# Performance work log

Measured on AMD Instinct MI355X. Metric: run time of the kernel, lower is better.

Reference implementation:

```python
import jax, jax.numpy as jnp
import numpy as np


def _mlp(x, W1, b1, W2, b2):
    # x: (B, M, T); torch MLPLayer: transpose(1,2) -> Linear -> Linear -> LeakyReLU -> transpose back
    h = jnp.einsum('bmt,hm->bht', x, W1) + b1[None, :, None]   # (B, H, T)
    y = jnp.einsum('bht,oh->bot', h, W2) + b2[None, :, None]   # (B, M, T)
    return jax.nn.leaky_relu(y, negative_slope=0.01)


def _calc_attn(q, k, v):
    # q: (B, M, Tq), k: (B, M, Tk), v: (B, M, Tk)
    Tq = q.shape[-1]
    qk = jnp.einsum('bmq,bmk->bqk', q, k)                       # (B, Tq, Tk)
    eye = jnp.eye(Tq, dtype=qk.dtype)                           # broadcasts: (Tq,Tq) or (1,1)
    logits = jnp.exp(qk - qk * eye / jnp.sqrt(jnp.asarray(Tq, qk.dtype)))
    scores = jax.nn.softmax(logits, axis=-1)
    return jnp.einsum('bqk,bmk->bmq', scores, v)                # (B, M, Tq)


def setup_inputs() -> dict:
    key = jax.random.key(0)
    B, M, T, H = 16, 128, 2048, 512
    ks = jax.random.split(key, 14)
    s = 0.02
    inp = {
        'pattern': jax.random.normal(ks[0], (B, M, T), jnp.float32),
        'value': jax.random.normal(ks[1], (B, M, T), jnp.float32),
        'kernel_size': 33,
    }
    names = ['q', 'k', 'o']
    for i, n in enumerate(names):
        inp['W%s1' % n] = jax.random.normal(ks[2 + 4 * i], (H, M), jnp.float32) * s
        inp['b%s1' % n] = jax.random.normal(ks[3 + 4 * i], (H,), jnp.float32) * s
        inp['W%s2' % n] = jax.random.normal(ks[4 + 4 * i], (M, H), jnp.float32) * s
        inp['b%s2' % n] = jax.random.normal(ks[5 + 4 * i], (M,), jnp.float32) * s
    return inp


def reference(pattern, value, kernel_size, Wq1, bq1, Wq2, bq2, Wk1, bk1, Wk2, bk2, Wo1, bo1, Wo2, bo2):
    query = _mlp(pattern, Wq1, bq1, Wq2, bq2)
    key = _mlp(pattern, Wk1, bk1, Wk2, bk2)
    # full (internal) attention
    attn_in = _calc_attn(query, key, value)                     # (B, M, T)
    rep_in = _mlp(attn_in, Wo1, bo1, Wo2, bo2)
    # windowed (external) attention
    T = query.shape[-1]
    cu = (kernel_size - 1) // 2
    q_w = query[..., T - 1 - cu : T - cu]                       # (B, M, 1)
    k_w = key[..., kernel_size - cu - 1 : T - cu - 2]           # (B, M, T-k-1)
    v_w = value[..., kernel_size : T - 1]                       # (B, M, T-k-1)
    attn_ex = _calc_attn(q_w, k_w, v_w)                         # (B, M, 1)
    rep_ex = _mlp(attn_ex, Wo1, bo1, Wo2, bo2)
    return jnp.concatenate([rep_in, rep_ex], axis=-1)           # (B, M, T+1)
```

## Files before the change

### kernel.cpp

```cpp
#include <hip/hip_runtime.h>
#include <hip/hip_bf16.h>
#include <math.h>

#define B_    16
#define M_    128
#define T_    2048
#define H_    512
#define TOUT_ 2049

typedef unsigned short u16;
typedef unsigned int   u32;
typedef __bf16 bf16x8 __attribute__((ext_vector_type(8)));
typedef float  f32x16 __attribute__((ext_vector_type(16)));
typedef float  f32x4  __attribute__((ext_vector_type(4)));
typedef u32    u32x4  __attribute__((ext_vector_type(4)));
typedef u32    u32x2  __attribute__((ext_vector_type(2)));

#define A_OFF     0
#define C_OFF     16384
#define MEAN_OFF  16896
#define AQKBF_OFF 19200
#define AOBF_OFF  35584
#define QT_OFF    43776
#define KT_OFF    (43776 + 2097152)
#define VB_OFF    (43776 + 2 * 2097152)

static __device__ __forceinline__ u16 f2bf(float f) {
  u32 u = __float_as_uint(f);
  u = (u + 0x7FFFu + ((u >> 16) & 1u)) >> 16;
  return (u16)u;
}
static __device__ __forceinline__ u32 pk2(float lo, float hi) {
  __hip_bfloat162 h = __float22bfloat162_rn(float2{lo, hi});
  u32 r;
  __builtin_memcpy(&r, &h, 4);
  return r;
}
static __device__ __forceinline__ bf16x8 ldfrag(const u16* p) {
  return __builtin_bit_cast(bf16x8, *(const u32x4*)p);
}
static __device__ __forceinline__ float ex2(float x) {
#if __has_builtin(__builtin_amdgcn_exp2f)
  return __builtin_amdgcn_exp2f(x);
#else
  return exp2f(x);
#endif
}

__global__ __launch_bounds__(128) void fuse_weights_all(
    const float* __restrict__ W1q, const float* __restrict__ b1q,
    const float* __restrict__ W2q, const float* __restrict__ b2q,
    const float* __restrict__ W1k, const float* __restrict__ b1k,
    const float* __restrict__ W2k, const float* __restrict__ b2k,
    const float* __restrict__ W1o, const float* __restrict__ b1o,
    const float* __restrict__ W2o, const float* __restrict__ b2o,
    float* __restrict__ A, float* __restrict__ c,
    u16* __restrict__ Aqk_bf, u16* __restrict__ Ao_bf) {
  __shared__ float w2row[H_];
  int which = blockIdx.x >> 7;
  int o = blockIdx.x & 127;
  const float* W1 = which == 0 ? W1q : which == 1 ? W1k : W1o;
  const float* b1 = which == 0 ? b1q : which == 1 ? b1k : b1o;
  const float* W2 = which == 0 ? W2q : which == 1 ? W2k : W2o;
  const float* b2 = which == 0 ? b2q : which == 1 ? b2k : b2o;
  int m = threadIdx.x;
  for (int h = m; h < H_; h += 128) w2row[h] = W2[o * H_ + h];
  __syncthreads();
  float acc = 0.f;
#pragma unroll 8
  for (int h = 0; h < H_; ++h) acc = fmaf(w2row[h], W1[h * M_ + m], acc);
  u16 ab = f2bf(acc);
  if (which == 0)      Aqk_bf[o * 128 + m] = ab;
  else if (which == 1) Aqk_bf[(128 + o) * 128 + m] = ab;
  else               { Ao_bf[o * 128 + m] = ab; A[o * M_ + m] = acc; }
  if (m < 64) {
    float cc = 0.f;
    for (int h = m; h < H_; h += 64) cc = fmaf(w2row[h], b1[h], cc);
#pragma unroll
    for (int off = 32; off > 0; off >>= 1) cc += __shfl_down(cc, off, 64);
    if (m == 0) c[which * 128 + o] = cc + b2[o];
  }
}

#define XS 68

__global__ __launch_bounds__(256) void prep_kernel(
    const float* __restrict__ pattern, const u16* __restrict__ Aqk_bf,
    const float* __restrict__ cqk, u16* __restrict__ qT, u16* __restrict__ kT,
    const float* __restrict__ value, u16* __restrict__ vb,
    float* __restrict__ meanv) {
  __shared__ alignas(16) float xsf[128 * XS];
  int bx = blockIdx.x;
  int tid = threadIdx.x;

  if (bx >= 512) {
    int bm = bx - 512;
    float* red = xsf;
    const float* row = value + (size_t)bm * T_;
    int i0 = tid * 8;
    float4 a = *(const float4*)(row + i0);
    float4 bq = *(const float4*)(row + i0 + 4);
    u32x4 o = {pk2(a.x, a.y), pk2(a.z, a.w), pk2(bq.x, bq.y), pk2(bq.z, bq.w)};
    *(u32x4*)&vb[(size_t)bm * T_ + i0] = o;
    float vals[8] = {a.x, a.y, a.z, a.w, bq.x, bq.y, bq.z, bq.w};
    float s = 0.f;
#pragma unroll
    for (int j = 0; j < 8; ++j) {
      int idx = i0 + j;
      if (idx >= 33 && idx < T_ - 1) s += vals[j];
    }
    red[tid] = s;
    __syncthreads();
    for (int st = 128; st > 0; st >>= 1) {
      if (tid < st) red[tid] += red[tid + st];
      __syncthreads();
    }
    if (tid == 0) meanv[bm] = red[0] * (1.f / 2014.f);
    return;
  }

  int b = bx >> 5;
  int t0 = (bx & 31) * 64;
  int lane = tid & 63;
  int wv = tid >> 6;
  int l31 = lane & 31;
  int lh8 = (lane >> 5) * 8;

  bf16x8 afr[2][8];
#pragma unroll
  for (int i = 0; i < 2; ++i) {
    const u16* ap = Aqk_bf + ((2 * wv + i) * 32 + l31) * 128 + lh8;
#pragma unroll
    for (int s = 0; s < 8; ++s) afr[i][s] = ldfrag(ap + 16 * s);
  }

#pragma unroll
  for (int rep = 0; rep < 8; ++rep) {
    int m = rep * 16 + (tid >> 4);
    int tc = (tid & 15) * 4;
    float4 v = *(const float4*)&pattern[(size_t)(b * M_ + m) * T_ + t0 + tc];
    *(float4*)&xsf[m * XS + tc] = v;
  }
  __syncthreads();

  bf16x8 bfr[2][8];
#pragma unroll
  for (int tt = 0; tt < 2; ++tt) {
#pragma unroll
    for (int s = 0; s < 8; ++s) {
      float v0 = xsf[(s * 16 + lh8 + 0) * XS + tt * 32 + l31];
      float v1 = xsf[(s * 16 + lh8 + 1) * XS + tt * 32 + l31];
      float v2 = xsf[(s * 16 + lh8 + 2) * XS + tt * 32 + l31];
      float v3 = xsf[(s * 16 + lh8 + 3) * XS + tt * 32 + l31];
      float v4 = xsf[(s * 16 + lh8 + 4) * XS + tt * 32 + l31];
      float v5 = xsf[(s * 16 + lh8 + 5) * XS + tt * 32 + l31];
      float v6 = xsf[(s * 16 + lh8 + 6) * XS + tt * 32 + l31];
      float v7 = xsf[(s * 16 + lh8 + 7) * XS + tt * 32 + l31];
      u32x4 p = {pk2(v0, v1), pk2(v2, v3), pk2(v4, v5), pk2(v6, v7)};
      bfr[tt][s] = __builtin_bit_cast(bf16x8, p);
    }
  }
  __syncthreads();

  u16* obuf = (u16*)xsf;
#pragma unroll
  for (int tt = 0; tt < 2; ++tt) {
#pragma unroll
    for (int i = 0; i < 2; ++i) {
      f32x16 acc;
#pragma unroll
      for (int r = 0; r < 16; ++r) acc[r] = 0.f;
#pragma unroll
      for (int s = 0; s < 8; ++s)
        acc = __builtin_amdgcn_mfma_f32_32x32x16_bf16(afr[i][s], bfr[tt][s], acc, 0, 0, 0);
      int ot = 2 * wv + i;
      int t = tt * 32 + l31;
      float sc = (ot < 4) ? 1.44269504f : 1.0f;
#pragma unroll
      for (int r = 0; r < 16; ++r) {
        int orow = (r & 3) + 8 * (r >> 2) + 4 * (lane >> 5);
        float v = acc[r] + cqk[ot * 32 + orow];
        v = v > 0.f ? v : 0.01f * v;
        obuf[t * 258 + ot * 32 + orow] = f2bf(v * sc);
      }
    }
  }
  __syncthreads();

  const u32* ob32 = (const u32*)obuf;
#pragma unroll
  for (int g = 0; g < 8; ++g) {
    int G = wv * 8 + g;
    int mat = G >> 4;
    int t = (G & 15) * 4 + (lane >> 4);
    int og2 = lane & 15;
    int wbase = t * 129 + mat * 64 + og2 * 4;
    u32x4 vv = {ob32[wbase], ob32[wbase + 1], ob32[wbase + 2], ob32[wbase + 3]};
    u32* dst = (u32*)((mat ? kT : qT) + ((size_t)(b * T_ + t0 + t)) * 128) + og2 * 4;
    *(u32x4*)dst = vv;
  }
}

#define QSTR 136
#define VSTR 72
#define NKT  (T_ / 64)
#define CINIT 0.52876637f

__global__ __launch_bounds__(256, 2) void attn_mfma_kernel(
    const u16* __restrict__ qT, const u16* __restrict__ kT,
    const u16* __restrict__ vB, const u16* __restrict__ Ao_bf,
    const float* __restrict__ co, const float* __restrict__ Aofp,
    const float* __restrict__ meanv, float* __restrict__ out) {
  extern __shared__ u16 smem[];
  u16* ks0 = smem;
  u16* ks1 = ks0 + 64 * QSTR;
  u16* vs0 = ks1 + 64 * QSTR;
  u16* vs1 = vs0 + 128 * VSTR;
  float* dls  = (float*)(vs1 + 128 * VSTR);
  float* pbuf = (float*)ks0;
  u16*   ptbuf = vs0;

  int b = blockIdx.y;
  int q0 = blockIdx.x * 64;
  int tid = threadIdx.x;
  int lane = tid & 63;
  int wv = tid >> 6;
  int l31 = lane & 31;
  int h = lane >> 5;
  int lh8 = h * 8;
  int qt = wv & 1;
  int kh = wv >> 1;

  const u16* gkb = kT + (size_t)b * T_ * 128;
  const u16* gvb = vB + (size_t)b * M_ * T_;
  int kr = tid >> 4, kc = (tid & 15) * 8;
  int vr = tid >> 3, vc = (tid & 7) * 8;

  u32x4 kreg[4], vreg[4];
#pragma unroll
  for (int it = 0; it < 4; ++it) {
    kreg[it] = *(const u32x4*)&gkb[(size_t)(it * 16 + kr) * 128 + kc];
    vreg[it] = *(const u32x4*)&gvb[(size_t)(it * 32 + vr) * T_ + vc];
  }

  bf16x8 qfrag[8];
  {
    const u16* qrow = qT + (size_t)(b * T_ + q0 + qt * 32 + l31) * 128 + lh8;
#pragma unroll
    for (int s = 0; s < 8; ++s) qfrag[s] = ldfrag(qrow + s * 16);
  }

#pragma unroll
  for (int it = 0; it < 4; ++it) {
    *(u32x4*)&ks0[(it * 16 + kr) * QSTR + kc] = kreg[it];
    *(u32x4*)&vs0[(it * 32 + vr) * VSTR + vc] = vreg[it];
  }
#pragma unroll
  for (int it = 0; it < 4; ++it) {
    kreg[it] = *(const u32x4*)&gkb[(size_t)(64 + it * 16 + kr) * 128 + kc];
    vreg[it] = *(const u32x4*)&gvb[(size_t)(it * 32 + vr) * T_ + 64 + vc];
  }

  f32x16 pacc[4];
  float den = 0.f;
#pragma unroll
  for (int i = 0; i < 16; ++i) {
    pacc[0][i] = 0.f; pacc[1][i] = 0.f; pacc[2][i] = 0.f; pacc[3][i] = 0.f;
  }

  for (int kt = 0; kt < NKT; ++kt) {
    int k0 = kt * 64;
    u16* kcur = (kt & 1) ? ks1 : ks0;
    u16* knxt = (kt & 1) ? ks0 : ks1;
    u16* vcur = (kt & 1) ? vs1 : vs0;
    u16* vnxt = (kt & 1) ? vs0 : vs1;
    __syncthreads();

    f32x16 sacc;
#pragma unroll
    for (int i = 0; i < 16; ++i) sacc[i] = CINIT;
    {
      const u16* krow = &kcur[(kh * 32 + l31) * QSTR + lh8];
      __builtin_amdgcn_s_setprio(1);
#pragma unroll
      for (int s = 0; s < 8; ++s) {
        bf16x8 kf = ldfrag(krow + s * 16);
        sacc = __builtin_amdgcn_mfma_f32_32x32x16_bf16(kf, qfrag[s], sacc, 0, 0, 0);
      }
      __builtin_amdgcn_s_setprio(0);
    }

    if (kt < NKT - 1) {
#pragma unroll
      for (int it = 0; it < 4; ++it) {
        *(u32x4*)&knxt[(it * 16 + kr) * QSTR + kc] = kreg[it];
        *(u32x4*)&vnxt[(it * 32 + vr) * VSTR + vc] = vreg[it];
      }
      int kn = (kt + 2 < NKT) ? (kt + 2) * 64 : (NKT - 1) * 64;
#pragma unroll
      for (int it = 0; it < 4; ++it) {
        kreg[it] = *(const u32x4*)&gkb[(size_t)(kn + it * 16 + kr) * 128 + kc];
        vreg[it] = *(const u32x4*)&gvb[(size_t)(it * 32 + vr) * T_ + kn + vc];
      }
    }

    if (k0 + kh * 32 == q0 + qt * 32) {
#pragma unroll
      for (int r = 0; r < 16; ++r) {
        int row = (r & 3) + 8 * (r >> 2) + 4 * h;
        if (row == l31) sacc[r] = fmaf(sacc[r], 0.97790291f, 0.01168420f);
      }
    }

    float w[16];
#pragma unroll
    for (int r = 0; r < 16; ++r) w[r] = ex2(ex2(sacc[r]));
    {
      float d0 = (w[0] + w[1]) + (w[2] + w[3]);
      float d1 = (w[4] + w[5]) + (w[6] + w[7]);
      float d2 = (w[8] + w[9]) + (w[10] + w[11]);
      float d3 = (w[12] + w[13]) + (w[14] + w[15]);
      den += (d0 + d1) + (d2 + d3);
    }
    u32 p00 = pk2(w[0], w[1]),  p01 = pk2(w[2], w[3]);
    u32 p10 = pk2(w[4], w[5]),  p11 = pk2(w[6], w[7]);
    u32 p20 = pk2(w[8], w[9]),  p21 = pk2(w[10], w[11]);
    u32 p30 = pk2(w[12], w[13]), p31 = pk2(w[14], w[15]);
    u32 e0 = __shfl_xor(h ? p00 : p10, 32, 64);
    u32 e1 = __shfl_xor(h ? p01 : p11, 32, 64);
    u32 e2 = __shfl_xor(h ? p20 : p30, 32, 64);
    u32 e3 = __shfl_xor(h ? p21 : p31, 32, 64);
    u32x4 f0 = h ? u32x4{e0, e1, p10, p11} : u32x4{p00, p01, e0, e1};
    u32x4 f1 = h ? u32x4{e2, e3, p30, p31} : u32x4{p20, p21, e2, e3};
    bf16x8 bw0 = __builtin_bit_cast(bf16x8, f0);
    bf16x8 bw1 = __builtin_bit_cast(bf16x8, f1);

    __builtin_amdgcn_s_setprio(1);
#pragma unroll
    for (int mt = 0; mt < 4; ++mt) {
      const u16* vrow = &vcur[(mt * 32 + l31) * VSTR + kh * 32 + lh8];
      bf16x8 vf0 = ldfrag(vrow);
      bf16x8 vf1 = ldfrag(vrow + 16);
      pacc[mt] = __builtin_amdgcn_mfma_f32_32x32x16_bf16(vf0, bw0, pacc[mt], 0, 0, 0);
      pacc[mt] = __builtin_amdgcn_mfma_f32_32x32x16_bf16(vf1, bw1, pacc[mt], 0, 0, 0);
    }
    __builtin_amdgcn_s_setprio(0);
  }

  float dq = den + __shfl_xor(den, 32, 64);

  __syncthreads();

  if (kh == 1) {
#pragma unroll
    for (int mt = 0; mt < 4; ++mt) {
      float* pb = &pbuf[((size_t)(qt * 4 + mt) * 64 + lane) * 16];
#pragma unroll
      for (int g = 0; g < 4; ++g) {
        f32x4 v = {pacc[mt][4 * g], pacc[mt][4 * g + 1],
                   pacc[mt][4 * g + 2], pacc[mt][4 * g + 3]};
        *(f32x4*)(pb + 4 * g) = v;
      }
    }
    if (lane < 32) dls[qt * 32 + lane] = dq;
  }
  __syncthreads();

  if (kh == 0) {
    float rden = 1.f / (dq + dls[qt * 32 + l31]);
#pragma unroll
    for (int mt = 0; mt < 4; ++mt) {
      const float* pb = &pbuf[((size_t)(qt * 4 + mt) * 64 + lane) * 16];
#pragma unroll
      for (int g = 0; g < 4; ++g) {
        f32x4 t = *(const f32x4*)(pb + 4 * g);
        float v0 = (pacc[mt][4 * g + 0] + t[0]) * rden;
        float v1 = (pacc[mt][4 * g + 1] + t[1]) * rden;
        float v2 = (pacc[mt][4 * g + 2] + t[2]) * rden;
        float v3 = (pacc[mt][4 * g + 3] + t[3]) * rden;
        int m0 = mt * 32 + 8 * g + 4 * h;
        u32x2 wp = {pk2(v0, v1), pk2(v2, v3)};
        *(u32x2*)&ptbuf[(qt * 32 + l31) * QSTR + m0] = wp;
      }
    }
  }
  __syncthreads();

  bf16x8 aofr[8];
  {
    const u16* ap = Ao_bf + (wv * 32 + l31) * 128 + lh8;
#pragma unroll
    for (int s = 0; s < 8; ++s) aofr[s] = ldfrag(ap + 16 * s);
  }
#pragma unroll
  for (int j = 0; j < 2; ++j) {
    bf16x8 pfr[8];
    const u16* pp = &ptbuf[(j * 32 + l31) * QSTR + lh8];
#pragma unroll
    for (int s = 0; s < 8; ++s) pfr[s] = ldfrag(pp + 16 * s);
    f32x16 oacc;
#pragma unroll
    for (int r = 0; r < 16; ++r) oacc[r] = 0.f;
#pragma unroll
    for (int s = 0; s < 8; ++s)
      oacc = __builtin_amdgcn_mfma_f32_32x32x16_bf16(aofr[s], pfr[s], oacc, 0, 0, 0);
#pragma unroll
    for (int r = 0; r < 16; ++r) {
      int orow = wv * 32 + (r & 3) + 8 * (r >> 2) + 4 * h;
      float v = oacc[r] + co[orow];
      v = v > 0.f ? v : 0.01f * v;
      out[((size_t)(b * M_ + orow)) * TOUT_ + q0 + j * 32 + l31] = v;
    }
  }

  if (blockIdx.x == 0 && tid < 128) {
    float acc = co[tid];
    const float* mv = meanv + b * 128;
    for (int m = 0; m < 128; ++m) acc = fmaf(Aofp[tid * 128 + m], mv[m], acc);
    acc = acc > 0.f ? acc : 0.01f * acc;
    out[((size_t)(b * M_ + tid)) * TOUT_ + 2048] = acc;
  }
}

extern "C" void kernel_launch(void* const* d_in, const int* in_sizes, int n_in,
                              void* d_out, int out_size, void* d_ws, size_t ws_size,
                              hipStream_t stream) {
  (void)in_sizes; (void)n_in; (void)out_size; (void)ws_size;
  const float* pattern = (const float*)d_in[0];
  const float* value   = (const float*)d_in[1];
  const float* Wq1 = (const float*)d_in[3];
  const float* bq1 = (const float*)d_in[4];
  const float* Wq2 = (const float*)d_in[5];
  const float* bq2 = (const float*)d_in[6];
  const float* Wk1 = (const float*)d_in[7];
  const float* bk1 = (const float*)d_in[8];
  const float* Wk2 = (const float*)d_in[9];
  const float* bk2 = (const float*)d_in[10];
  const float* Wo1 = (const float*)d_in[11];
  const float* bo1 = (const float*)d_in[12];
  const float* Wo2 = (const float*)d_in[13];
  const float* bo2 = (const float*)d_in[14];

  float* ws     = (float*)d_ws;
  float* A      = ws + A_OFF;
  float* c      = ws + C_OFF;
  float* meanv  = ws + MEAN_OFF;
  u16*   Aqk_bf = (u16*)(ws + AQKBF_OFF);
  u16*   Ao_bf  = (u16*)(ws + AOBF_OFF);
  u16*   qT     = (u16*)(ws + QT_OFF);
  u16*   kT     = (u16*)(ws + KT_OFF);
  u16*   vB     = (u16*)(ws + VB_OFF);
  float* out    = (float*)d_out;

  fuse_weights_all<<<384, 128, 0, stream>>>(
      Wq1, bq1, Wq2, bq2, Wk1, bk1, Wk2, bk2, Wo1, bo1, Wo2, bo2,
      A, c, Aqk_bf, Ao_bf);

  prep_kernel<<<512 + B_ * M_, 256, 0, stream>>>(
      pattern, Aqk_bf, c, qT, kT, value, vB, meanv);

  size_t lds_bytes = (size_t)(2 * 64 * QSTR + 2 * 128 * VSTR) * 2 + 64 * 4;
  attn_mfma_kernel<<<dim3(T_ / 64, B_), 256, lds_bytes, stream>>>(
      qT, kT, vB, Ao_bf, c + 256, A, meanv, out);
}
```

Baseline: 196.9 us.

## Double attention query/key tile to 128 with 512-thread blocks

The attention kernel now processes 128 queries per block with 8 waves, and each loop iteration covers 128 keys. Each wave computes two 32x32 score tiles per step. This halves how often K/V tiles are streamed per query and gives more independent MFMA work in each iteration. In exchange, LDS use roughly doubles, so only one block fits per CU. The grid shrinks to 256 blocks, and register pressure under launch_bounds(512,2) may force spills.

Measured after the change: 190.1 us. -3.4%, faster.

```diff
diff --git a/kernel.cpp b/kernel.cpp
--- a/kernel.cpp
+++ b/kernel.cpp
@@ -202,46 +202,39 @@
 }
 
 #define QSTR 136
-#define VSTR 72
-#define NKT  (T_ / 64)
+#define VSTR 136
+#define KTILE 128
+#define NKT  (T_ / KTILE)
 #define CINIT 0.52876637f
 
-__global__ __launch_bounds__(256, 2) void attn_mfma_kernel(
+__global__ __launch_bounds__(512, 2) void attn_mfma_kernel(
     const u16* __restrict__ qT, const u16* __restrict__ kT,
     const u16* __restrict__ vB, const u16* __restrict__ Ao_bf,
     const float* __restrict__ co, const float* __restrict__ Aofp,
     const float* __restrict__ meanv, float* __restrict__ out) {
   extern __shared__ u16 smem[];
   u16* ks0 = smem;
-  u16* ks1 = ks0 + 64 * QSTR;
-  u16* vs0 = ks1 + 64 * QSTR;
+  u16* ks1 = ks0 + 128 * QSTR;
+  u16* vs0 = ks1 + 128 * QSTR;
   u16* vs1 = vs0 + 128 * VSTR;
   float* dls  = (float*)(vs1 + 128 * VSTR);
   float* pbuf = (float*)ks0;
   u16*   ptbuf = vs0;
 
   int b = blockIdx.y;
-  int q0 = blockIdx.x * 64;
+  int q0 = blockIdx.x * 128;
   int tid = threadIdx.x;
   int lane = tid & 63;
   int wv = tid >> 6;
   int l31 = lane & 31;
   int h = lane >> 5;
   int lh8 = h * 8;
-  int qt = wv & 1;
-  int kh = wv >> 1;
+  int qt = wv & 3;
+  int kh = wv >> 2;
 
   const u16* gkb = kT + (size_t)b * T_ * 128;
   const u16* gvb = vB + (size_t)b * M_ * T_;
   int kr = tid >> 4, kc = (tid & 15) * 8;
-  int vr = tid >> 3, vc = (tid & 7) * 8;
-
-  u32x4 kreg[4], vreg[4];
-#pragma unroll
-  for (int it = 0; it < 4; ++it) {
-    kreg[it] = *(const u32x4*)&gkb[(size_t)(it * 16 + kr) * 128 + kc];
-    vreg[it] = *(const u32x4*)&gvb[(size_t)(it * 32 + vr) * T_ + vc];
-  }
 
   bf16x8 qfrag[8];
   {
@@ -250,15 +243,21 @@
     for (int s = 0; s < 8; ++s) qfrag[s] = ldfrag(qrow + s * 16);
   }
 
+  u32x4 kreg[4], vreg[4];
 #pragma unroll
   for (int it = 0; it < 4; ++it) {
-    *(u32x4*)&ks0[(it * 16 + kr) * QSTR + kc] = kreg[it];
-    *(u32x4*)&vs0[(it * 32 + vr) * VSTR + vc] = vreg[it];
+    kreg[it] = *(const u32x4*)&gkb[(size_t)(it * 32 + kr) * 128 + kc];
+    vreg[it] = *(const u32x4*)&gvb[(size_t)(it * 32 + kr) * T_ + kc];
   }
 #pragma unroll
   for (int it = 0; it < 4; ++it) {
-    kreg[it] = *(const u32x4*)&gkb[(size_t)(64 + it * 16 + kr) * 128 + kc];
-    vreg[it] = *(const u32x4*)&gvb[(size_t)(it * 32 + vr) * T_ + 64 + vc];
+    *(u32x4*)&ks0[(it * 32 + kr) * QSTR + kc] = kreg[it];
+    *(u32x4*)&vs0[(it * 32 + kr) * VSTR + kc] = vreg[it];
+  }
+#pragma unroll
+  for (int it = 0; it < 4; ++it) {
+    kreg[it] = *(const u32x4*)&gkb[(size_t)(KTILE + it * 32 + kr) * 128 + kc];
+    vreg[it] = *(const u32x4*)&gvb[(size_t)(it * 32 + kr) * T_ + KTILE + kc];
   }
 
   f32x16 pacc[4];
@@ -269,23 +268,29 @@
   }
 
   for (int kt = 0; kt < NKT; ++kt) {
-    int k0 = kt * 64;
+    int k0 = kt * KTILE;
     u16* kcur = (kt & 1) ? ks1 : ks0;
     u16* knxt = (kt & 1) ? ks0 : ks1;
     u16* vcur = (kt & 1) ? vs1 : vs0;
     u16* vnxt = (kt & 1) ? vs0 : vs1;
     __syncthreads();
 
-    f32x16 sacc;
-#pragma unroll
-    for (int i = 0; i < 16; ++i) sacc[i] = CINIT;
+    f32x16 sacc_a, sacc_b;
+#pragma unroll
+    for (int i = 0; i < 16; ++i) { sacc_a[i] = CINIT; sacc_b[i] = CINIT; }
     {
-      const u16* krow = &kcur[(kh * 32 + l31) * QSTR + lh8];
+      const u16* krowa = &kcur[(kh * 64 + l31) * QSTR + lh8];
+      const u16* krowb = krowa + 32 * QSTR;
       __builtin_amdgcn_s_setprio(1);
 #pragma unroll
       for (int s = 0; s < 8; ++s) {
-        bf16x8 kf = ldfrag(krow + s * 16);
-        sacc = __builtin_amdgcn_mfma_f32_32x32x16_bf16(kf, qfrag[s], sacc, 0, 0, 0);
+        bf16x8 kfa = ldfrag(krowa + s * 16);
+        sacc_a = __builtin_amdgcn_mfma_f32_32x32x16_bf16(kfa, qfrag[s], sacc_a, 0, 0, 0);
+      }
+#pragma unroll
+      for (int s = 0; s < 8; ++s) {
+        bf16x8 kfb = ldfrag(krowb + s * 16);
+        sacc_b = __builtin_amdgcn_mfma_f32_32x32x16_bf16(kfb, qfrag[s], sacc_b, 0, 0, 0);
       }
       __builtin_amdgcn_s_setprio(0);
     }
@@ -293,58 +298,95 @@
     if (kt < NKT - 1) {
 #pragma unroll
       for (int it = 0; it < 4; ++it) {
-        *(u32x4*)&knxt[(it * 16 + kr) * QSTR + kc] = kreg[it];
-        *(u32x4*)&vnxt[(it * 32 + vr) * VSTR + vc] = vreg[it];
-      }
-      int kn = (kt + 2 < NKT) ? (kt + 2) * 64 : (NKT - 1) * 64;
+        *(u32x4*)&knxt[(it * 32 + kr) * QSTR + kc] = kreg[it];
+        *(u32x4*)&vnxt[(it * 32 + kr) * VSTR + kc] = vreg[it];
+      }
+      int kn = (kt + 2 < NKT) ? (kt + 2) * KTILE : (NKT - 1) * KTILE;
 #pragma unroll
       for (int it = 0; it < 4; ++it) {
-        kreg[it] = *(const u32x4*)&gkb[(size_t)(kn + it * 16 + kr) * 128 + kc];
-        vreg[it] = *(const u32x4*)&gvb[(size_t)(it * 32 + vr) * T_ + kn + vc];
-      }
-    }
-
-    if (k0 + kh * 32 == q0 + qt * 32) {
+        kreg[it] = *(const u32x4*)&gkb[(size_t)(kn + it * 32 + kr) * 128 + kc];
+        vreg[it] = *(const u32x4*)&gvb[(size_t)(it * 32 + kr) * T_ + kn + kc];
+      }
+    }
+
+    if (k0 + kh * 64 == q0 + qt * 32) {
 #pragma unroll
       for (int r = 0; r < 16; ++r) {
         int row = (r & 3) + 8 * (r >> 2) + 4 * h;
-        if (row == l31) sacc[r] = fmaf(sacc[r], 0.97790291f, 0.01168420f);
-      }
-    }
-
-    float w[16];
-#pragma unroll
-    for (int r = 0; r < 16; ++r) w[r] = ex2(ex2(sacc[r]));
+        if (row == l31) sacc_a[r] = fmaf(sacc_a[r], 0.97790291f, 0.01168420f);
+      }
+    } else if (k0 + kh * 64 + 32 == q0 + qt * 32) {
+#pragma unroll
+      for (int r = 0; r < 16; ++r) {
+        int row = (r & 3) + 8 * (r >> 2) + 4 * h;
+        if (row == l31) sacc_b[r] = fmaf(sacc_b[r], 0.97790291f, 0.01168420f);
+      }
+    }
+
     {
+      float w[16];
+#pragma unroll
+      for (int r = 0; r < 16; ++r) w[r] = ex2(ex2(sacc_a[r]));
       float d0 = (w[0] + w[1]) + (w[2] + w[3]);
       float d1 = (w[4] + w[5]) + (w[6] + w[7]);
       float d2 = (w[8] + w[9]) + (w[10] + w[11]);
       float d3 = (w[12] + w[13]) + (w[14] + w[15]);
       den += (d0 + d1) + (d2 + d3);
-    }
-    u32 p00 = pk2(w[0], w[1]),  p01 = pk2(w[2], w[3]);
-    u32 p10 = pk2(w[4], w[5]),  p11 = pk2(w[6], w[7]);
-    u32 p20 = pk2(w[8], w[9]),  p21 = pk2(w[10], w[11]);
-    u32 p30 = pk2(w[12], w[13]), p31 = pk2(w[14], w[15]);
-    u32 e0 = __shfl_xor(h ? p00 : p10, 32, 64);
-    u32 e1 = __shfl_xor(h ? p01 : p11, 32, 64);
-    u32 e2 = __shfl_xor(h ? p20 : p30, 32, 64);
-    u32 e3 = __shfl_xor(h ? p21 : p31, 32, 64);
-    u32x4 f0 = h ? u32x4{e0, e1, p10, p11} : u32x4{p00, p01, e0, e1};
-    u32x4 f1 = h ? u32x4{e2, e3, p30, p31} : u32x4{p20, p21, e2, e3};
-    bf16x8 bw0 = __builtin_bit_cast(bf16x8, f0);
-    bf16x8 bw1 = __builtin_bit_cast(bf16x8, f1);
-
-    __builtin_amdgcn_s_setprio(1);
-#pragma unroll
-    for (int mt = 0; mt < 4; ++mt) {
-      const u16* vrow = &vcur[(mt * 32 + l31) * VSTR + kh * 32 + lh8];
-      bf16x8 vf0 = ldfrag(vrow);
-      bf16x8 vf1 = ldfrag(vrow + 16);
-      pacc[mt] = __builtin_amdgcn_mfma_f32_32x32x16_bf16(vf0, bw0, pacc[mt], 0, 0, 0);
-      pacc[mt] = __builtin_amdgcn_mfma_f32_32x32x16_bf16(vf1, bw1, pacc[mt], 0, 0, 0);
-    }
-    __builtin_amdgcn_s_setprio(0);
+      u32 p00 = pk2(w[0], w[1]),  p01 = pk2(w[2], w[3]);
+      u32 p10 = pk2(w[4], w[5]),  p11 = pk2(w[6], w[7]);
+      u32 p20 = pk2(w[8], w[9]),  p21 = pk2(w[10], w[11]);
+      u32 p30 = pk2(w[12], w[13]), p31 = pk2(w[14], w[15]);
+      u32 e0 = __shfl_xor(h ? p00 : p10, 32, 64);
+      u32 e1 = __shfl_xor(h ? p01 : p11, 32, 64);
+      u32 e2 = __shfl_xor(h ? p20 : p30, 32, 64);
+      u32 e3 = __shfl_xor(h ? p21 : p31, 32, 64);
+      u32x4 f0 = h ? u32x4{e0, e1, p10, p11} : u32x4{p00, p01, e0, e1};
+      u32x4 f1 = h ? u32x4{e2, e3, p30, p31} : u32x4{p20, p21, e2, e3};
+      bf16x8 bw0 = __builtin_bit_cast(bf16x8, f0);
+      bf16x8 bw1 = __builtin_bit_cast(bf16x8, f1);
+      __builtin_amdgcn_s_setprio(1);
+#pragma unroll
+      for (int mt = 0; mt < 4; ++mt) {
+        const u16* vrow = &vcur[(mt * 32 + l31) * VSTR + kh * 64 + lh8];
+        bf16x8 vf0 = ldfrag(vrow);
+        bf16x8 vf1 = ldfrag(vrow + 16);
+        pacc[mt] = __builtin_amdgcn_mfma_f32_32x32x16_bf16(vf0, bw0, pacc[mt], 0, 0, 0);
+        pacc[mt] = __builtin_amdgcn_mfma_f32_32x32x16_bf16(vf1, bw1, pacc[mt], 0, 0, 0);
+      }
+      __builtin_amdgcn_s_setprio(0);
+    }
+    {
+      float w[16];
+#pragma unroll
+      for (int r = 0; r < 16; ++r) w[r] = ex2(ex2(sacc_b[r]));
+      float d0 = (w[0] + w[1]) + (w[2] + w[3]);
+      float d1 = (w[4] + w[5]) + (w[6] + w[7]);
+      float d2 = (w[8] + w[9]) + (w[10] + w[11]);
+      float d3 = (w[12] + w[13]) + (w[14] + w[15]);
+      den += (d0 + d1) + (d2 + d3);
+      u32 p00 = pk2(w[0], w[1]),  p01 = pk2(w[2], w[3]);
+      u32 p10 = pk2(w[4], w[5]),  p11 = pk2(w[6], w[7]);
+      u32 p20 = pk2(w[8], w[9]),  p21 = pk2(w[10], w[11]);
+      u32 p30 = pk2(w[12], w[13]), p31 = pk2(w[14], w[15]);
+      u32 e0 = __shfl_xor(h ? p00 : p10, 32, 64);
+      u32 e1 = __shfl_xor(h ? p01 : p11, 32, 64);
+      u32 e2 = __shfl_xor(h ? p20 : p30, 32, 64);
+      u32 e3 = __shfl_xor(h ? p21 : p31, 32, 64);
+      u32x4 f0 = h ? u32x4{e0, e1, p10, p11} : u32x4{p00, p01, e0, e1};
+      u32x4 f1 = h ? u32x4{e2, e3, p30, p31} : u32x4{p20, p21, e2, e3};
+      bf16x8 bw2 = __builtin_bit_cast(bf16x8, f0);
+      bf16x8 bw3 = __builtin_bit_cast(bf16x8, f1);
+      __builtin_amdgcn_s_setprio(1);
+#pragma unroll
+      for (int mt = 0; mt < 4; ++mt) {
+        const u16* vrow = &vcur[(mt * 32 + l31) * VSTR + kh * 64 + 32 + lh8];
+        bf16x8 vf2 = ldfrag(vrow);
+        bf16x8 vf3 = ldfrag(vrow + 16);
+        pacc[mt] = __builtin_amdgcn_mfma_f32_32x32x16_bf16(vf2, bw2, pacc[mt], 0, 0, 0);
+        pacc[mt] = __builtin_amdgcn_mfma_f32_32x32x16_bf16(vf3, bw3, pacc[mt], 0, 0, 0);
+      }
+      __builtin_amdgcn_s_setprio(0);
+    }
   }
 
   float dq = den + __shfl_xor(den, 32, 64);
@@ -388,14 +430,15 @@
 
   bf16x8 aofr[8];
   {
-    const u16* ap = Ao_bf + (wv * 32 + l31) * 128 + lh8;
+    const u16* ap = Ao_bf + ((wv & 3) * 32 + l31) * 128 + lh8;
 #pragma unroll
     for (int s = 0; s < 8; ++s) aofr[s] = ldfrag(ap + 16 * s);
   }
 #pragma unroll
   for (int j = 0; j < 2; ++j) {
+    int qt2 = kh * 2 + j;
     bf16x8 pfr[8];
-    const u16* pp = &ptbuf[(j * 32 + l31) * QSTR + lh8];
+    const u16* pp = &ptbuf[(qt2 * 32 + l31) * QSTR + lh8];
 #pragma unroll
     for (int s = 0; s < 8; ++s) pfr[s] = ldfrag(pp + 16 * s);
     f32x16 oacc;
@@ -406,10 +449,10 @@
       oacc = __builtin_amdgcn_mfma_f32_32x32x16_bf16(aofr[s], pfr[s], oacc, 0, 0, 0);
 #pragma unroll
     for (int r = 0; r < 16; ++r) {
-      int orow = wv * 32 + (r & 3) + 8 * (r >> 2) + 4 * h;
+      int orow = (wv & 3) * 32 + (r & 3) + 8 * (r >> 2) + 4 * h;
       float v = oacc[r] + co[orow];
       v = v > 0.f ? v : 0.01f * v;
-      out[((size_t)(b * M_ + orow)) * TOUT_ + q0 + j * 32 + l31] = v;
+      out[((size_t)(b * M_ + orow)) * TOUT_ + q0 + qt2 * 32 + l31] = v;
     }
   }
 
@@ -459,7 +502,7 @@
   prep_kernel<<<512 + B_ * M_, 256, 0, stream>>>(
       pattern, Aqk_bf, c, qT, kT, value, vB, meanv);
 
-  size_t lds_bytes = (size_t)(2 * 64 * QSTR + 2 * 128 * VSTR) * 2 + 64 * 4;
-  attn_mfma_kernel<<<dim3(T_ / 64, B_), 256, lds_bytes, stream>>>(
+  size_t lds_bytes = (size_t)(2 * 128 * QSTR + 2 * 128 * VSTR) * 2 + 128 * 4;
+  attn_mfma_kernel<<<dim3(T_ / 128, B_), 512, lds_bytes, stream>>>(
       qT, kT, vB, Ao_bf, c + 256, A, meanv, out);
 }
```

## Enlarge attention blocks to 128 queries with 16 waves sharing K/V tiles

Applied to the files above, without the earlier changes.

Each attention block now has 1024 threads and covers 128 queries instead of 64. Each K/V tile staged in LDS is therefore reused by four query tiles, halving global K/V traffic per query. The PV accumulation is split across two M-halves, so each score tile's QK^T MFMAs and exponentials are computed twice, by both M-half waves. The s_setprio hints are removed. The grid shrinks to 256 blocks using about 99KB of LDS each, which lowers occupancy, and launch_bounds(1024,4) may pressure registers.

Result: slower. 210.2 us (+6.8%).

```diff
diff --git a/kernel.cpp b/kernel.cpp
--- a/kernel.cpp
+++ b/kernel.cpp
@@ -203,46 +203,41 @@
 
 #define QSTR 136
 #define VSTR 72
-#define NKT  (T_ / 64)
+#define KTILE 64
+#define NKT  (T_ / KTILE)
 #define CINIT 0.52876637f
 
-__global__ __launch_bounds__(256, 2) void attn_mfma_kernel(
+__global__ __launch_bounds__(1024, 4) void attn_mfma_kernel(
     const u16* __restrict__ qT, const u16* __restrict__ kT,
     const u16* __restrict__ vB, const u16* __restrict__ Ao_bf,
     const float* __restrict__ co, const float* __restrict__ Aofp,
     const float* __restrict__ meanv, float* __restrict__ out) {
   extern __shared__ u16 smem[];
   u16* ks0 = smem;
-  u16* ks1 = ks0 + 64 * QSTR;
-  u16* vs0 = ks1 + 64 * QSTR;
-  u16* vs1 = vs0 + 128 * VSTR;
-  float* dls  = (float*)(vs1 + 128 * VSTR);
-  float* pbuf = (float*)ks0;
-  u16*   ptbuf = vs0;
+  u16* ks1 = smem + 8704;
+  u16* vs0 = smem + 17408;
+  u16* vs1 = smem + 26624;
+  float* pbuf  = (float*)smem;
+  u16*   ptbuf = smem + 33024;
+  float* dls   = (float*)(smem + 50432);
 
   int b = blockIdx.y;
-  int q0 = blockIdx.x * 64;
+  int q0 = blockIdx.x * 128;
   int tid = threadIdx.x;
   int lane = tid & 63;
   int wv = tid >> 6;
   int l31 = lane & 31;
   int h = lane >> 5;
   int lh8 = h * 8;
-  int qt = wv & 1;
-  int kh = wv >> 1;
+  int qt = wv & 3;
+  int kh = (wv >> 2) & 1;
+  int mh = wv >> 3;
 
   const u16* gkb = kT + (size_t)b * T_ * 128;
   const u16* gvb = vB + (size_t)b * M_ * T_;
   int kr = tid >> 4, kc = (tid & 15) * 8;
   int vr = tid >> 3, vc = (tid & 7) * 8;
 
-  u32x4 kreg[4], vreg[4];
-#pragma unroll
-  for (int it = 0; it < 4; ++it) {
-    kreg[it] = *(const u32x4*)&gkb[(size_t)(it * 16 + kr) * 128 + kc];
-    vreg[it] = *(const u32x4*)&gvb[(size_t)(it * 32 + vr) * T_ + vc];
-  }
-
   bf16x8 qfrag[8];
   {
     const u16* qrow = qT + (size_t)(b * T_ + q0 + qt * 32 + l31) * 128 + lh8;
@@ -250,61 +245,47 @@
     for (int s = 0; s < 8; ++s) qfrag[s] = ldfrag(qrow + s * 16);
   }
 
-#pragma unroll
-  for (int it = 0; it < 4; ++it) {
-    *(u32x4*)&ks0[(it * 16 + kr) * QSTR + kc] = kreg[it];
-    *(u32x4*)&vs0[(it * 32 + vr) * VSTR + vc] = vreg[it];
-  }
-#pragma unroll
-  for (int it = 0; it < 4; ++it) {
-    kreg[it] = *(const u32x4*)&gkb[(size_t)(64 + it * 16 + kr) * 128 + kc];
-    vreg[it] = *(const u32x4*)&gvb[(size_t)(it * 32 + vr) * T_ + 64 + vc];
-  }
-
-  f32x16 pacc[4];
+  u32x4 kreg, vreg;
+  kreg = *(const u32x4*)&gkb[(size_t)kr * 128 + kc];
+  vreg = *(const u32x4*)&gvb[(size_t)vr * T_ + vc];
+  *(u32x4*)&ks0[kr * QSTR + kc] = kreg;
+  *(u32x4*)&vs0[vr * VSTR + vc] = vreg;
+  kreg = *(const u32x4*)&gkb[(size_t)(KTILE + kr) * 128 + kc];
+  vreg = *(const u32x4*)&gvb[(size_t)vr * T_ + KTILE + vc];
+
+  f32x16 pacc[2];
   float den = 0.f;
 #pragma unroll
-  for (int i = 0; i < 16; ++i) {
-    pacc[0][i] = 0.f; pacc[1][i] = 0.f; pacc[2][i] = 0.f; pacc[3][i] = 0.f;
-  }
+  for (int i = 0; i < 16; ++i) { pacc[0][i] = 0.f; pacc[1][i] = 0.f; }
 
   for (int kt = 0; kt < NKT; ++kt) {
-    int k0 = kt * 64;
     u16* kcur = (kt & 1) ? ks1 : ks0;
     u16* knxt = (kt & 1) ? ks0 : ks1;
     u16* vcur = (kt & 1) ? vs1 : vs0;
     u16* vnxt = (kt & 1) ? vs0 : vs1;
     __syncthreads();
 
+    if (kt < NKT - 1) {
+      *(u32x4*)&knxt[kr * QSTR + kc] = kreg;
+      *(u32x4*)&vnxt[vr * VSTR + vc] = vreg;
+      int kn = (kt + 2 < NKT) ? (kt + 2) * KTILE : (NKT - 1) * KTILE;
+      kreg = *(const u32x4*)&gkb[(size_t)(kn + kr) * 128 + kc];
+      vreg = *(const u32x4*)&gvb[(size_t)vr * T_ + kn + vc];
+    }
+
     f32x16 sacc;
 #pragma unroll
     for (int i = 0; i < 16; ++i) sacc[i] = CINIT;
     {
       const u16* krow = &kcur[(kh * 32 + l31) * QSTR + lh8];
-      __builtin_amdgcn_s_setprio(1);
 #pragma unroll
       for (int s = 0; s < 8; ++s) {
         bf16x8 kf = ldfrag(krow + s * 16);
         sacc = __builtin_amdgcn_mfma_f32_32x32x16_bf16(kf, qfrag[s], sacc, 0, 0, 0);
       }
-      __builtin_amdgcn_s_setprio(0);
-    }
-
-    if (kt < NKT - 1) {
-#pragma unroll
-      for (int it = 0; it < 4; ++it) {
-        *(u32x4*)&knxt[(it * 16 + kr) * QSTR + kc] = kreg[it];
-        *(u32x4*)&vnxt[(it * 32 + vr) * VSTR + vc] = vreg[it];
-      }
-      int kn = (kt + 2 < NKT) ? (kt + 2) * 64 : (NKT - 1) * 64;
-#pragma unroll
-      for (int it = 0; it < 4; ++it) {
-        kreg[it] = *(const u32x4*)&gkb[(size_t)(kn + it * 16 + kr) * 128 + kc];
-        vreg[it] = *(const u32x4*)&gvb[(size_t)(it * 32 + vr) * T_ + kn + vc];
-      }
-    }
-
-    if (k0 + kh * 32 == q0 + qt * 32) {
+    }
+
+    if (kt * KTILE + kh * 32 == q0 + qt * 32) {
 #pragma unroll
       for (int r = 0; r < 16; ++r) {
         int row = (r & 3) + 8 * (r >> 2) + 4 * h;
@@ -335,16 +316,15 @@
     bf16x8 bw0 = __builtin_bit_cast(bf16x8, f0);
     bf16x8 bw1 = __builtin_bit_cast(bf16x8, f1);
 
-    __builtin_amdgcn_s_setprio(1);
-#pragma unroll
-    for (int mt = 0; mt < 4; ++mt) {
-      const u16* vrow = &vcur[(mt * 32 + l31) * VSTR + kh * 32 + lh8];
+#pragma unroll
+    for (int i = 0; i < 2; ++i) {
+      int mtg = mh * 2 + i;
+      const u16* vrow = &vcur[(mtg * 32 + l31) * VSTR + kh * 32 + lh8];
       bf16x8 vf0 = ldfrag(vrow);
       bf16x8 vf1 = ldfrag(vrow + 16);
-      pacc[mt] = __builtin_amdgcn_mfma_f32_32x32x16_bf16(vf0, bw0, pacc[mt], 0, 0, 0);
-      pacc[mt] = __builtin_amdgcn_mfma_f32_32x32x16_bf16(vf1, bw1, pacc[mt], 0, 0, 0);
-    }
-    __builtin_amdgcn_s_setprio(0);
+      pacc[i] = __builtin_amdgcn_mfma_f32_32x32x16_bf16(vf0, bw0, pacc[i], 0, 0, 0);
+      pacc[i] = __builtin_amdgcn_mfma_f32_32x32x16_bf16(vf1, bw1, pacc[i], 0, 0, 0);
+    }
   }
 
   float dq = den + __shfl_xor(den, 32, 64);
@@ -353,32 +333,32 @@
 
   if (kh == 1) {
 #pragma unroll
-    for (int mt = 0; mt < 4; ++mt) {
-      float* pb = &pbuf[((size_t)(qt * 4 + mt) * 64 + lane) * 16];
+    for (int i = 0; i < 2; ++i) {
+      float* pb = &pbuf[(((qt * 2 + mh) * 2 + i) * 64 + lane) * 16];
 #pragma unroll
       for (int g = 0; g < 4; ++g) {
-        f32x4 v = {pacc[mt][4 * g], pacc[mt][4 * g + 1],
-                   pacc[mt][4 * g + 2], pacc[mt][4 * g + 3]};
+        f32x4 v = {pacc[i][4 * g], pacc[i][4 * g + 1],
+                   pacc[i][4 * g + 2], pacc[i][4 * g + 3]};
         *(f32x4*)(pb + 4 * g) = v;
       }
     }
-    if (lane < 32) dls[qt * 32 + lane] = dq;
+    if (mh == 0 && lane < 32) dls[qt * 32 + lane] = dq;
   }
   __syncthreads();
 
   if (kh == 0) {
     float rden = 1.f / (dq + dls[qt * 32 + l31]);
 #pragma unroll
-    for (int mt = 0; mt < 4; ++mt) {
-      const float* pb = &pbuf[((size_t)(qt * 4 + mt) * 64 + lane) * 16];
+    for (int i = 0; i < 2; ++i) {
+      const float* pb = &pbuf[(((qt * 2 + mh) * 2 + i) * 64 + lane) * 16];
 #pragma unroll
       for (int g = 0; g < 4; ++g) {
         f32x4 t = *(const f32x4*)(pb + 4 * g);
-        float v0 = (pacc[mt][4 * g + 0] + t[0]) * rden;
-        float v1 = (pacc[mt][4 * g + 1] + t[1]) * rden;
-        float v2 = (pacc[mt][4 * g + 2] + t[2]) * rden;
-        float v3 = (pacc[mt][4 * g + 3] + t[3]) * rden;
-        int m0 = mt * 32 + 8 * g + 4 * h;
+        float v0 = (pacc[i][4 * g + 0] + t[0]) * rden;
+        float v1 = (pacc[i][4 * g + 1] + t[1]) * rden;
+        float v2 = (pacc[i][4 * g + 2] + t[2]) * rden;
+        float v3 = (pacc[i][4 * g + 3] + t[3]) * rden;
+        int m0 = (mh * 2 + i) * 32 + 8 * g + 4 * h;
         u32x2 wp = {pk2(v0, v1), pk2(v2, v3)};
         *(u32x2*)&ptbuf[(qt * 32 + l31) * QSTR + m0] = wp;
       }
@@ -388,14 +368,14 @@
 
   bf16x8 aofr[8];
   {
-    const u16* ap = Ao_bf + (wv * 32 + l31) * 128 + lh8;
+    const u16* ap = Ao_bf + ((wv & 3) * 32 + l31) * 128 + lh8;
 #pragma unroll
     for (int s = 0; s < 8; ++s) aofr[s] = ldfrag(ap + 16 * s);
   }
-#pragma unroll
-  for (int j = 0; j < 2; ++j) {
+  {
+    int qt2 = wv >> 2;
     bf16x8 pfr[8];
-    const u16* pp = &ptbuf[(j * 32 + l31) * QSTR + lh8];
+    const u16* pp = &ptbuf[(qt2 * 32 + l31) * QSTR + lh8];
 #pragma unroll
     for (int s = 0; s < 8; ++s) pfr[s] = ldfrag(pp + 16 * s);
     f32x16 oacc;
@@ -406,10 +386,10 @@
       oacc = __builtin_amdgcn_mfma_f32_32x32x16_bf16(aofr[s], pfr[s], oacc, 0, 0, 0);
 #pragma unroll
     for (int r = 0; r < 16; ++r) {
-      int orow = wv * 32 + (r & 3) + 8 * (r >> 2) + 4 * h;
+      int orow = (wv & 3) * 32 + (r & 3) + 8 * (r >> 2) + 4 * h;
       float v = oacc[r] + co[orow];
       v = v > 0.f ? v : 0.01f * v;
-      out[((size_t)(b * M_ + orow)) * TOUT_ + q0 + j * 32 + l31] = v;
+      out[((size_t)(b * M_ + orow)) * TOUT_ + q0 + qt2 * 32 + l31] = v;
     }
   }
 
@@ -459,7 +439,7 @@
   prep_kernel<<<512 + B_ * M_, 256, 0, stream>>>(
       pattern, Aqk_bf, c, qT, kT, value, vB, meanv);
 
-  size_t lds_bytes = (size_t)(2 * 64 * QSTR + 2 * 128 * VSTR) * 2 + 64 * 4;
-  attn_mfma_kernel<<<dim3(T_ / 64, B_), 256, lds_bytes, stream>>>(
+  size_t lds_bytes = 101376;
+  attn_mfma_kernel<<<dim3(T_ / 128, B_), 1024, lds_bytes, stream>>>(
       qT, kT, vB, Ao_bf, c + 256, A, meanv, out);
 }
```

## Enlarge attention tiles to 128 queries and 128 keys with 1024-thread blocks

Applied to the files above, without the earlier changes.

The attention kernel now handles 128 queries per block with 16 waves (4 query tiles × 4 key splits) and loads 128-key K/V tiles into LDS, halving the grid. This raises reuse of each K/V tile across more queries and cuts global K/V reloads, at the cost of a two-stage cross-wave reduction of partial outputs and denominators through LDS. It also uses much more LDS per block (~138 KB), so only one block fits per CU, and it drops the s_setprio hints. Prefetch stores are moved before the QK MFMAs.

Measured after the change: 252.0 us. +28.0%, slower.

```diff
diff --git a/kernel.cpp b/kernel.cpp
--- a/kernel.cpp
+++ b/kernel.cpp
@@ -202,46 +202,40 @@
 }
 
 #define QSTR 136
-#define VSTR 72
-#define NKT  (T_ / 64)
+#define VSTR 136
+#define KTILE 128
+#define NKT  (T_ / KTILE)
 #define CINIT 0.52876637f
 
-__global__ __launch_bounds__(256, 2) void attn_mfma_kernel(
+__global__ __launch_bounds__(1024) void attn_mfma_kernel(
     const u16* __restrict__ qT, const u16* __restrict__ kT,
     const u16* __restrict__ vB, const u16* __restrict__ Ao_bf,
     const float* __restrict__ co, const float* __restrict__ Aofp,
     const float* __restrict__ meanv, float* __restrict__ out) {
   extern __shared__ u16 smem[];
   u16* ks0 = smem;
-  u16* ks1 = ks0 + 64 * QSTR;
-  u16* vs0 = ks1 + 64 * QSTR;
-  u16* vs1 = vs0 + 128 * VSTR;
-  float* dls  = (float*)(vs1 + 128 * VSTR);
-  float* pbuf = (float*)ks0;
-  u16*   ptbuf = vs0;
+  u16* ks1 = smem + 17408;
+  u16* vs0 = smem + 34816;
+  u16* vs1 = smem + 52224;
+  float* pbuf  = (float*)smem;
+  u16*   ptbuf = smem + 32768;
+  float* dls   = (float*)(smem + 69632);
 
   int b = blockIdx.y;
-  int q0 = blockIdx.x * 64;
+  int q0 = blockIdx.x * 128;
   int tid = threadIdx.x;
   int lane = tid & 63;
   int wv = tid >> 6;
   int l31 = lane & 31;
   int h = lane >> 5;
   int lh8 = h * 8;
-  int qt = wv & 1;
-  int kh = wv >> 1;
+  int qt = wv & 3;
+  int ks = wv >> 2;
 
   const u16* gkb = kT + (size_t)b * T_ * 128;
   const u16* gvb = vB + (size_t)b * M_ * T_;
-  int kr = tid >> 4, kc = (tid & 15) * 8;
-  int vr = tid >> 3, vc = (tid & 7) * 8;
-
-  u32x4 kreg[4], vreg[4];
-#pragma unroll
-  for (int it = 0; it < 4; ++it) {
-    kreg[it] = *(const u32x4*)&gkb[(size_t)(it * 16 + kr) * 128 + kc];
-    vreg[it] = *(const u32x4*)&gvb[(size_t)(it * 32 + vr) * T_ + vc];
-  }
+  int sr = tid >> 3;
+  int sc = (tid & 7) * 16;
 
   bf16x8 qfrag[8];
   {
@@ -250,16 +244,19 @@
     for (int s = 0; s < 8; ++s) qfrag[s] = ldfrag(qrow + s * 16);
   }
 
-#pragma unroll
-  for (int it = 0; it < 4; ++it) {
-    *(u32x4*)&ks0[(it * 16 + kr) * QSTR + kc] = kreg[it];
-    *(u32x4*)&vs0[(it * 32 + vr) * VSTR + vc] = vreg[it];
-  }
-#pragma unroll
-  for (int it = 0; it < 4; ++it) {
-    kreg[it] = *(const u32x4*)&gkb[(size_t)(64 + it * 16 + kr) * 128 + kc];
-    vreg[it] = *(const u32x4*)&gvb[(size_t)(it * 32 + vr) * T_ + 64 + vc];
-  }
+  u32x4 kreg[2], vreg[2];
+  kreg[0] = *(const u32x4*)&gkb[(size_t)sr * 128 + sc];
+  kreg[1] = *(const u32x4*)&gkb[(size_t)sr * 128 + sc + 8];
+  vreg[0] = *(const u32x4*)&gvb[(size_t)sr * T_ + sc];
+  vreg[1] = *(const u32x4*)&gvb[(size_t)sr * T_ + sc + 8];
+  *(u32x4*)&ks0[sr * QSTR + sc] = kreg[0];
+  *(u32x4*)&ks0[sr * QSTR + sc + 8] = kreg[1];
+  *(u32x4*)&vs0[sr * VSTR + sc] = vreg[0];
+  *(u32x4*)&vs0[sr * VSTR + sc + 8] = vreg[1];
+  kreg[0] = *(const u32x4*)&gkb[(size_t)(KTILE + sr) * 128 + sc];
+  kreg[1] = *(const u32x4*)&gkb[(size_t)(KTILE + sr) * 128 + sc + 8];
+  vreg[0] = *(const u32x4*)&gvb[(size_t)sr * T_ + KTILE + sc];
+  vreg[1] = *(const u32x4*)&gvb[(size_t)sr * T_ + KTILE + sc + 8];
 
   f32x16 pacc[4];
   float den = 0.f;
@@ -269,42 +266,37 @@
   }
 
   for (int kt = 0; kt < NKT; ++kt) {
-    int k0 = kt * 64;
     u16* kcur = (kt & 1) ? ks1 : ks0;
     u16* knxt = (kt & 1) ? ks0 : ks1;
     u16* vcur = (kt & 1) ? vs1 : vs0;
     u16* vnxt = (kt & 1) ? vs0 : vs1;
     __syncthreads();
 
+    if (kt < NKT - 1) {
+      *(u32x4*)&knxt[sr * QSTR + sc] = kreg[0];
+      *(u32x4*)&knxt[sr * QSTR + sc + 8] = kreg[1];
+      *(u32x4*)&vnxt[sr * VSTR + sc] = vreg[0];
+      *(u32x4*)&vnxt[sr * VSTR + sc + 8] = vreg[1];
+      int kn = (kt + 2 < NKT) ? (kt + 2) * KTILE : (NKT - 1) * KTILE;
+      kreg[0] = *(const u32x4*)&gkb[(size_t)(kn + sr) * 128 + sc];
+      kreg[1] = *(const u32x4*)&gkb[(size_t)(kn + sr) * 128 + sc + 8];
+      vreg[0] = *(const u32x4*)&gvb[(size_t)sr * T_ + kn + sc];
+      vreg[1] = *(const u32x4*)&gvb[(size_t)sr * T_ + kn + sc + 8];
+    }
+
     f32x16 sacc;
 #pragma unroll
     for (int i = 0; i < 16; ++i) sacc[i] = CINIT;
     {
-      const u16* krow = &kcur[(kh * 32 + l31) * QSTR + lh8];
-      __builtin_amdgcn_s_setprio(1);
+      const u16* krow = &kcur[(ks * 32 + l31) * QSTR + lh8];
 #pragma unroll
       for (int s = 0; s < 8; ++s) {
         bf16x8 kf = ldfrag(krow + s * 16);
         sacc = __builtin_amdgcn_mfma_f32_32x32x16_bf16(kf, qfrag[s], sacc, 0, 0, 0);
       }
-      __builtin_amdgcn_s_setprio(0);
-    }
-
-    if (kt < NKT - 1) {
-#pragma unroll
-      for (int it = 0; it < 4; ++it) {
-        *(u32x4*)&knxt[(it * 16 + kr) * QSTR + kc] = kreg[it];
-        *(u32x4*)&vnxt[(it * 32 + vr) * VSTR + vc] = vreg[it];
-      }
-      int kn = (kt + 2 < NKT) ? (kt + 2) * 64 : (NKT - 1) * 64;
-#pragma unroll
-      for (int it = 0; it < 4; ++it) {
-        kreg[it] = *(const u32x4*)&gkb[(size_t)(kn + it * 16 + kr) * 128 + kc];
-        vreg[it] = *(const u32x4*)&gvb[(size_t)(it * 32 + vr) * T_ + kn + vc];
-      }
-    }
-
-    if (k0 + kh * 32 == q0 + qt * 32) {
+    }
+
+    if (kt * KTILE + ks * 32 == q0 + qt * 32) {
 #pragma unroll
       for (int r = 0; r < 16; ++r) {
         int row = (r & 3) + 8 * (r >> 2) + 4 * h;
@@ -335,45 +327,77 @@
     bf16x8 bw0 = __builtin_bit_cast(bf16x8, f0);
     bf16x8 bw1 = __builtin_bit_cast(bf16x8, f1);
 
-    __builtin_amdgcn_s_setprio(1);
 #pragma unroll
     for (int mt = 0; mt < 4; ++mt) {
-      const u16* vrow = &vcur[(mt * 32 + l31) * VSTR + kh * 32 + lh8];
+      const u16* vrow = &vcur[(mt * 32 + l31) * VSTR + ks * 32 + lh8];
       bf16x8 vf0 = ldfrag(vrow);
       bf16x8 vf1 = ldfrag(vrow + 16);
       pacc[mt] = __builtin_amdgcn_mfma_f32_32x32x16_bf16(vf0, bw0, pacc[mt], 0, 0, 0);
       pacc[mt] = __builtin_amdgcn_mfma_f32_32x32x16_bf16(vf1, bw1, pacc[mt], 0, 0, 0);
     }
-    __builtin_amdgcn_s_setprio(0);
   }
 
   float dq = den + __shfl_xor(den, 32, 64);
 
   __syncthreads();
 
-  if (kh == 1) {
+  if (ks != 0 && lane < 32) dls[ks * 128 + qt * 32 + l31] = dq;
+  if (ks & 1) {
+    int sidx = ks >> 1;
 #pragma unroll
     for (int mt = 0; mt < 4; ++mt) {
-      float* pb = &pbuf[((size_t)(qt * 4 + mt) * 64 + lane) * 16];
+      float* pb = &pbuf[(((sidx * 4 + qt) * 4 + mt) << 10)];
 #pragma unroll
       for (int g = 0; g < 4; ++g) {
         f32x4 v = {pacc[mt][4 * g], pacc[mt][4 * g + 1],
                    pacc[mt][4 * g + 2], pacc[mt][4 * g + 3]};
-        *(f32x4*)(pb + 4 * g) = v;
-      }
-    }
-    if (lane < 32) dls[qt * 32 + lane] = dq;
-  }
-  __syncthreads();
-
-  if (kh == 0) {
-    float rden = 1.f / (dq + dls[qt * 32 + l31]);
+        *(f32x4*)(pb + (g << 8) + lane * 4) = v;
+      }
+    }
+  }
+  __syncthreads();
+
+  if (!(ks & 1)) {
+    int sidx = ks >> 1;
 #pragma unroll
     for (int mt = 0; mt < 4; ++mt) {
-      const float* pb = &pbuf[((size_t)(qt * 4 + mt) * 64 + lane) * 16];
+      const float* pb = &pbuf[(((sidx * 4 + qt) * 4 + mt) << 10)];
 #pragma unroll
       for (int g = 0; g < 4; ++g) {
-        f32x4 t = *(const f32x4*)(pb + 4 * g);
+        f32x4 t = *(const f32x4*)(pb + (g << 8) + lane * 4);
+        pacc[mt][4 * g]     += t[0];
+        pacc[mt][4 * g + 1] += t[1];
+        pacc[mt][4 * g + 2] += t[2];
+        pacc[mt][4 * g + 3] += t[3];
+      }
+    }
+  }
+  __syncthreads();
+
+  if (ks == 2) {
+#pragma unroll
+    for (int mt = 0; mt < 4; ++mt) {
+      float* pb = &pbuf[((qt * 4 + mt) << 10)];
+#pragma unroll
+      for (int g = 0; g < 4; ++g) {
+        f32x4 v = {pacc[mt][4 * g], pacc[mt][4 * g + 1],
+                   pacc[mt][4 * g + 2], pacc[mt][4 * g + 3]};
+        *(f32x4*)(pb + (g << 8) + lane * 4) = v;
+      }
+    }
+  }
+  __syncthreads();
+
+  if (ks == 0) {
+    float dtot = dq + dls[128 + qt * 32 + l31] + dls[256 + qt * 32 + l31]
+               + dls[384 + qt * 32 + l31];
+    float rden = 1.f / dtot;
+#pragma unroll
+    for (int mt = 0; mt < 4; ++mt) {
+      const float* pb = &pbuf[((qt * 4 + mt) << 10)];
+#pragma unroll
+      for (int g = 0; g < 4; ++g) {
+        f32x4 t = *(const f32x4*)(pb + (g << 8) + lane * 4);
         float v0 = (pacc[mt][4 * g + 0] + t[0]) * rden;
         float v1 = (pacc[mt][4 * g + 1] + t[1]) * rden;
         float v2 = (pacc[mt][4 * g + 2] + t[2]) * rden;
@@ -388,14 +412,14 @@
 
   bf16x8 aofr[8];
   {
-    const u16* ap = Ao_bf + (wv * 32 + l31) * 128 + lh8;
+    const u16* ap = Ao_bf + ((wv & 3) * 32 + l31) * 128 + lh8;
 #pragma unroll
     for (int s = 0; s < 8; ++s) aofr[s] = ldfrag(ap + 16 * s);
   }
-#pragma unroll
-  for (int j = 0; j < 2; ++j) {
+  {
+    int qt2 = wv >> 2;
     bf16x8 pfr[8];
-    const u16* pp = &ptbuf[(j * 32 + l31) * QSTR + lh8];
+    const u16* pp = &ptbuf[(qt2 * 32 + l31) * QSTR + lh8];
 #pragma unroll
     for (int s = 0; s < 8; ++s) pfr[s] = ldfrag(pp + 16 * s);
     f32x16 oacc;
@@ -406,10 +430,10 @@
       oacc = __builtin_amdgcn_mfma_f32_32x32x16_bf16(aofr[s], pfr[s], oacc, 0, 0, 0);
 #pragma unroll
     for (int r = 0; r < 16; ++r) {
-      int orow = wv * 32 + (r & 3) + 8 * (r >> 2) + 4 * h;
+      int orow = (wv & 3) * 32 + (r & 3) + 8 * (r >> 2) + 4 * h;
       float v = oacc[r] + co[orow];
       v = v > 0.f ? v : 0.01f * v;
-      out[((size_t)(b * M_ + orow)) * TOUT_ + q0 + j * 32 + l31] = v;
+      out[((size_t)(b * M_ + orow)) * TOUT_ + q0 + qt2 * 32 + l31] = v;
     }
   }
 
@@ -459,7 +483,7 @@
   prep_kernel<<<512 + B_ * M_, 256, 0, stream>>>(
       pattern, Aqk_bf, c, qT, kT, value, vB, meanv);
 
-  size_t lds_bytes = (size_t)(2 * 64 * QSTR + 2 * 128 * VSTR) * 2 + 64 * 4;
-  attn_mfma_kernel<<<dim3(T_ / 64, B_), 256, lds_bytes, stream>>>(
+  size_t lds_bytes = 141312;
+  attn_mfma_kernel<<<dim3(T_ / 128, B_), 1024, lds_bytes, stream>>>(
       qT, kT, vB, Ao_bf, c + 256, A, meanv, out);
 }
```
